# Kernel tuning notes

Measured on AMD Instinct MI355X. Metric: run time of the kernel, lower is better.

The kernel has to match this reference:

```python
import jax, jax.numpy as jnp
import numpy as np

T, B, D, H = 1024, 256, 128, 256

def setup_inputs() -> dict:
    key = jax.random.key(0)
    ks = jax.random.split(key, 6)
    s = 1.0 / np.sqrt(H)
    return {
        "x": jax.random.normal(ks[0], (T, B, D), dtype=jnp.float32),
        "delta_ts": jax.random.uniform(ks[1], (B, T), dtype=jnp.float32) * 10.0,  # elapsed times > 0
        "h0": jnp.zeros((B, H), dtype=jnp.float32),
        "c0": jnp.zeros((B, H), dtype=jnp.float32),
        "W": jax.random.normal(ks[2], (4 * H, D), dtype=jnp.float32) * s,
        "U": jax.random.normal(ks[3], (4 * H, H), dtype=jnp.float32) * s,
        "b": jnp.zeros((4 * H,), dtype=jnp.float32),
        "Wd": jax.random.normal(ks[4], (H, H), dtype=jnp.float32) * s,
        "bd": jnp.zeros((H,), dtype=jnp.float32),
    }

def reference(x, delta_ts, h0, c0, W, U, b, Wd, bd):
    """Time-aware LSTM (T-LSTM, Baytas et al. 2017) layer over time-major input.
    x: [T,B,D], delta_ts: [B,T]. Returns (outputs [T,B,H], (h,c))."""
    e = jnp.float32(np.e)

    def step(carry, inp):
        h, c = carry                 # [B,H] each
        xt, dt = inp                 # [B,D], [B]
        # memory decomposition with elapsed-time discount g(dt)=1/log(e+dt)
        Cs = jnp.tanh(c @ Wd.T + bd)                     # short-term memory [B,H]
        Cs_hat = Cs * (1.0 / jnp.log(e + dt))[:, None]   # discounted short-term
        c_star = c - Cs + Cs_hat                          # adjusted previous cell
        gates = xt @ W.T + h @ U.T + b                    # [B,4H]
        i, f, g, o = jnp.split(gates, 4, axis=-1)
        c_new = jax.nn.sigmoid(f) * c_star + jax.nn.sigmoid(i) * jnp.tanh(g)
        h_new = jax.nn.sigmoid(o) * jnp.tanh(c_new)
        return (h_new, c_new), h_new

    (h, c), outs = jax.lax.scan(step, (h0, c0), (x, delta_ts.T))
    return outs, h, c
```

## Files before the change

kernel.cpp:

```cpp
#include <hip/hip_runtime.h>

#define T_STEPS 1024
#define BATCH   256
#define DIM     128
#define HID     256
#define NSLICE  8
#define BT      16
#define NGROUP  (BATCH / BT)
#define NBLOCK  (NGROUP * NSLICE)
#define JW      (HID / NSLICE)

#define U_OFF    0
#define W_OFF    65536
#define WD_OFF   98304
#define H_OFF    114688
#define C_OFF    122880
#define GST_OFF  131072
#define CS0_OFF  139520
#define CS1_OFF  141632
#define SMEM_TOTAL 143744

typedef float f32x4 __attribute__((ext_vector_type(4)));
typedef short bf16x8 __attribute__((ext_vector_type(8)));

__device__ __forceinline__ unsigned short f2bf(float f) {
    union { float f; unsigned u; } v; v.f = f;
    unsigned r = (v.u + 0x7fffu + ((v.u >> 16) & 1u)) >> 16;
    return (unsigned short)r;
}
__device__ __forceinline__ float sigm(float v) { return 1.0f / (1.0f + __expf(-v)); }
__device__ __forceinline__ float tanh_fast(float v) {
    const float e = __expf(2.0f * v);
    return 1.0f - 2.0f / (e + 1.0f);
}

__global__ __launch_bounds__(512)
void tlstm_kernel(const float* __restrict__ x,
                  const float* __restrict__ dts,
                  const float* __restrict__ h0,
                  const float* __restrict__ c0,
                  const float* __restrict__ W,
                  const float* __restrict__ U,
                  const float* __restrict__ bvec,
                  const float* __restrict__ Wd,
                  const float* __restrict__ bd,
                  float* __restrict__ out,
                  unsigned long long* pbuf)
{
    extern __shared__ char smem[];
    float* gates_st = (float*)(smem + GST_OFF);
    float* cs0      = (float*)(smem + CS0_OFF);
    float* cs1      = (float*)(smem + CS1_OFF);

    const int tid = threadIdx.x;
    const int g  = blockIdx.x / NSLICE;
    const int s  = blockIdx.x % NSLICE;
    const int bb = g * BT;
    const int jb = s * JW;

    const int lane = tid & 63;
    const int wid  = tid >> 6;
    const int lrow = lane & 15;
    const int lkg  = lane >> 4;
    const int n0   = wid << 4;

    const int b_ = tid >> 5;
    const int jj = tid & 31;

    for (int idx = tid; idx < 128 * 256; idx += 512) {
        const int r = idx >> 8, k = idx & 255;
        const int urow = ((r >> 5) * HID) + jb + (r & 31);
        int bo = (r << 9) + (k << 1); bo ^= (r & 7) << 4;
        *(unsigned short*)(smem + U_OFF + bo) = f2bf(U[(size_t)urow * HID + k]);
    }
    for (int idx = tid; idx < 128 * 128; idx += 512) {
        const int r = idx >> 7, k = idx & 127;
        const int wrow = ((r >> 5) * HID) + jb + (r & 31);
        int bo = (r << 8) + (k << 1); bo ^= (r & 7) << 4;
        *(unsigned short*)(smem + W_OFF + bo) = f2bf(W[(size_t)wrow * DIM + k]);
    }
    for (int idx = tid; idx < 32 * 256; idx += 512) {
        const int r = idx >> 8, k = idx & 255;
        int bo = (r << 9) + (k << 1); bo ^= (r & 7) << 4;
        *(unsigned short*)(smem + WD_OFF + bo) = f2bf(Wd[(size_t)(jb + r) * HID + k]);
    }

    const float bI = bvec[jb + jj];
    const float bF = bvec[HID + jb + jj];
    const float bG = bvec[2 * HID + jb + jj];
    const float bO = bvec[3 * HID + jb + jj];
    const float bD = bd[jb + jj];

    float4 xr[8];
    float dt_cur;
    {
        const float* xp = x + ((size_t)0 * BATCH + bb + lrow) * DIM + (lkg << 3);
        #pragma unroll
        for (int kc = 0; kc < 4; ++kc) {
            xr[2 * kc]     = *(const float4*)(xp + kc * 32);
            xr[2 * kc + 1] = *(const float4*)(xp + kc * 32 + 4);
        }
        dt_cur = dts[(size_t)(bb + b_) * T_STEPS + 0];
    }

    float c_reg;
    {
        const float h0v = h0[(size_t)(bb + b_) * HID + jb + jj];
        const float c0v = c0[(size_t)(bb + b_) * HID + jb + jj];
        c_reg = c0v;
        const unsigned long long pv = (1ull << 32)
            | ((unsigned)f2bf(h0v) << 16) | (unsigned)f2bf(c0v);
        const size_t ei = (((size_t)0 * NGROUP + g) * NSLICE + s) * 512 + b_ * 32 + jj;
        __hip_atomic_store(pbuf + ei, pv, __ATOMIC_RELAXED, __HIP_MEMORY_SCOPE_AGENT);
    }

    for (int t = 0; t < T_STEPS; ++t) {
        const int cur = t & 1;

        bf16x8 xa[4];
        #pragma unroll
        for (int kc = 0; kc < 4; ++kc) {
            const float4 f0 = xr[2 * kc];
            const float4 f1 = xr[2 * kc + 1];
            bf16x8 a;
            a[0] = (short)f2bf(f0.x); a[1] = (short)f2bf(f0.y);
            a[2] = (short)f2bf(f0.z); a[3] = (short)f2bf(f0.w);
            a[4] = (short)f2bf(f1.x); a[5] = (short)f2bf(f1.y);
            a[6] = (short)f2bf(f1.z); a[7] = (short)f2bf(f1.w);
            xa[kc] = a;
        }
        f32x4 accX = {0.f, 0.f, 0.f, 0.f};
        {
            const int wr = n0 + lrow;
            #pragma unroll
            for (int kc = 0; kc < 4; ++kc) {
                int wo = (wr << 8) + ((kc * 32 + (lkg << 3)) << 1); wo ^= (wr & 7) << 4;
                const bf16x8 wv = *(const bf16x8*)(smem + W_OFF + wo);
                accX = __builtin_amdgcn_mfma_f32_16x16x32_bf16(xa[kc], wv, accX, 0, 0, 0);
            }
        }

        unsigned long long v[8];
        {
            const unsigned target = (unsigned)(t + 1);
            const unsigned long long* sp = pbuf
                + (((size_t)cur * NGROUP + g) * NSLICE + wid) * 512
                + ((lane >> 2) * 32 + ((lane & 3) << 3));
            bool ok;
            do {
                #pragma unroll
                for (int i = 0; i < 8; ++i)
                    v[i] = __hip_atomic_load(sp + i, __ATOMIC_RELAXED, __HIP_MEMORY_SCOPE_AGENT);
                ok = true;
                #pragma unroll
                for (int i = 0; i < 8; ++i)
                    ok = ok && ((unsigned)(v[i] >> 32) == target);
            } while (!__all((int)ok));
        }

        {
            bf16x8 hv, cv;
            #pragma unroll
            for (int i = 0; i < 8; ++i) {
                hv[i] = (short)((unsigned short)(v[i] >> 16));
                cv[i] = (short)((unsigned short)(v[i] & 0xffffu));
            }
            const int r  = lane >> 2;
            const int cb = (wid << 6) + ((lane & 3) << 4);
            int bo = (r << 9) + cb; bo ^= (r & 7) << 4;
            *(bf16x8*)(smem + H_OFF + bo) = hv;
            *(bf16x8*)(smem + C_OFF + bo) = cv;
        }
        __syncthreads();

        f32x4 accH = {0.f, 0.f, 0.f, 0.f};
        {
            const int wr = n0 + lrow;
            #pragma unroll
            for (int kc = 0; kc < 8; ++kc) {
                int ao = (lrow << 9) + ((kc * 32 + (lkg << 3)) << 1); ao ^= (lrow & 7) << 4;
                const bf16x8 av = *(const bf16x8*)(smem + H_OFF + ao);
                int uo = (wr << 9) + ((kc * 32 + (lkg << 3)) << 1); uo ^= (wr & 7) << 4;
                const bf16x8 uv = *(const bf16x8*)(smem + U_OFF + uo);
                accH = __builtin_amdgcn_mfma_f32_16x16x32_bf16(av, uv, accH, 0, 0, 0);
            }
        }
        if (wid < 4) {
            f32x4 accC = {0.f, 0.f, 0.f, 0.f};
            const int nt = wid >> 1;
            const int kh = wid & 1;
            const int wr = (nt << 4) + lrow;
            #pragma unroll
            for (int kc = 0; kc < 4; ++kc) {
                const int kk = kh * 4 + kc;
                int ao = (lrow << 9) + ((kk * 32 + (lkg << 3)) << 1); ao ^= (lrow & 7) << 4;
                const bf16x8 av = *(const bf16x8*)(smem + C_OFF + ao);
                int wo = (wr << 9) + ((kk * 32 + (lkg << 3)) << 1); wo ^= (wr & 7) << 4;
                const bf16x8 wv = *(const bf16x8*)(smem + WD_OFF + wo);
                accC = __builtin_amdgcn_mfma_f32_16x16x32_bf16(av, wv, accC, 0, 0, 0);
            }
            float* dst = kh ? cs1 : cs0;
            #pragma unroll
            for (int i = 0; i < 4; ++i)
                dst[((lkg << 2) + i) * 33 + (nt << 4) + lrow] = accC[i];
        }
        #pragma unroll
        for (int i = 0; i < 4; ++i)
            gates_st[((lkg << 2) + i) * 132 + n0 + lrow] = accX[i] + accH[i];

        __syncthreads();

        float cn, hn;
        {
            const float ipre = gates_st[b_ * 132 + jj]      + bI;
            const float fpre = gates_st[b_ * 132 + 32 + jj] + bF;
            const float gpre = gates_st[b_ * 132 + 64 + jj] + bG;
            const float opre = gates_st[b_ * 132 + 96 + jj] + bO;
            const float cspre = cs0[b_ * 33 + jj] + cs1[b_ * 33 + jj] + bD;
            const float gdt  = 1.0f / __logf(2.718281828459045f + dt_cur);
            const float Cs    = tanh_fast(cspre);
            const float cstar = c_reg - Cs + Cs * gdt;
            cn = sigm(fpre) * cstar + sigm(ipre) * tanh_fast(gpre);
            hn = sigm(opre) * tanh_fast(cn);
            c_reg = cn;
        }

        if (t == T_STEPS - 1) {
            out[((size_t)t * BATCH + bb + b_) * HID + jb + jj] = hn;
            const size_t base = (size_t)T_STEPS * BATCH * HID;
            out[base + (size_t)(bb + b_) * HID + jb + jj] = hn;
            out[base + (size_t)BATCH * HID + (size_t)(bb + b_) * HID + jb + jj] = cn;
            break;
        }

        {
            const unsigned long long pv = ((unsigned long long)(unsigned)(t + 2) << 32)
                | ((unsigned)f2bf(hn) << 16) | (unsigned)f2bf(cn);
            const size_t ei = (((size_t)(cur ^ 1) * NGROUP + g) * NSLICE + s) * 512
                            + b_ * 32 + jj;
            __hip_atomic_store(pbuf + ei, pv, __ATOMIC_RELAXED, __HIP_MEMORY_SCOPE_AGENT);
        }

        out[((size_t)t * BATCH + bb + b_) * HID + jb + jj] = hn;
        {
            const float* xp = x + ((size_t)(t + 1) * BATCH + bb + lrow) * DIM + (lkg << 3);
            #pragma unroll
            for (int kc = 0; kc < 4; ++kc) {
                xr[2 * kc]     = *(const float4*)(xp + kc * 32);
                xr[2 * kc + 1] = *(const float4*)(xp + kc * 32 + 4);
            }
            dt_cur = dts[(size_t)(bb + b_) * T_STEPS + (t + 1)];
        }
    }
}

extern "C" void kernel_launch(void* const* d_in, const int* in_sizes, int n_in,
                              void* d_out, int out_size, void* d_ws, size_t ws_size,
                              hipStream_t stream) {
    (void)in_sizes; (void)n_in; (void)out_size; (void)ws_size;
    const float* x   = (const float*)d_in[0];
    const float* dts = (const float*)d_in[1];
    const float* h0  = (const float*)d_in[2];
    const float* c0  = (const float*)d_in[3];
    const float* W   = (const float*)d_in[4];
    const float* U   = (const float*)d_in[5];
    const float* bv  = (const float*)d_in[6];
    const float* Wd  = (const float*)d_in[7];
    const float* bd  = (const float*)d_in[8];
    float* out = (float*)d_out;

    unsigned long long* pbuf = (unsigned long long*)d_ws;
    const size_t pbuf_bytes = 2ull * NGROUP * NSLICE * 512 * 8;

    hipMemsetAsync(pbuf, 0, pbuf_bytes, stream);
    hipFuncSetAttribute((const void*)tlstm_kernel,
                        hipFuncAttributeMaxDynamicSharedMemorySize, SMEM_TOTAL);
    tlstm_kernel<<<dim3(NBLOCK), dim3(512), SMEM_TOTAL, stream>>>(
        x, dts, h0, c0, W, U, bv, Wd, bd, out, pbuf);
}
```

Measured before the change: 5.439 ms.

## Interleave two batch sub-tiles per block to overlap cross-block sync latency

```diff
diff --git a/kernel.cpp b/kernel.cpp
--- a/kernel.cpp
+++ b/kernel.cpp
@@ -4,10 +4,10 @@
 #define BATCH   256
 #define DIM     128
 #define HID     256
+#define NGP     8
 #define NSLICE  8
+#define NBLOCK  (NGP * NSLICE)
 #define BT      16
-#define NGROUP  (BATCH / BT)
-#define NBLOCK  (NGROUP * NSLICE)
 #define JW      (HID / NSLICE)
 
 #define U_OFF    0
@@ -20,6 +20,11 @@
 #define CS1_OFF  141632
 #define SMEM_TOTAL 143744
 
+#define SLICE_CH 512
+#define ST_CH    (8 * SLICE_CH)
+#define GP_CH    (2 * ST_CH)
+#define BUF_CH   (NGP * GP_CH)
+
 typedef float f32x4 __attribute__((ext_vector_type(4)));
 typedef short bf16x8 __attribute__((ext_vector_type(8)));
 
@@ -32,6 +37,17 @@
 __device__ __forceinline__ float tanh_fast(float v) {
     const float e = __expf(2.0f * v);
     return 1.0f - 2.0f / (e + 1.0f);
+}
+__device__ __forceinline__ void lgkm_bar() {
+    asm volatile("s_waitcnt lgkmcnt(0)" ::: "memory");
+    __builtin_amdgcn_s_barrier();
+    __builtin_amdgcn_sched_barrier(0);
+}
+__device__ __forceinline__ void probe8(const unsigned long long* sp, unsigned long long v[8]) {
+    #pragma unroll
+    for (int i = 0; i < 8; ++i)
+        v[i] = __hip_atomic_load(sp + i, __ATOMIC_RELAXED, __HIP_MEMORY_SCOPE_AGENT);
+    __builtin_amdgcn_sched_barrier(0);
 }
 
 __global__ __launch_bounds__(512)
@@ -52,12 +68,7 @@
     float* cs0      = (float*)(smem + CS0_OFF);
     float* cs1      = (float*)(smem + CS1_OFF);
 
-    const int tid = threadIdx.x;
-    const int g  = blockIdx.x / NSLICE;
-    const int s  = blockIdx.x % NSLICE;
-    const int bb = g * BT;
-    const int jb = s * JW;
-
+    const int tid  = threadIdx.x;
     const int lane = tid & 63;
     const int wid  = tid >> 6;
     const int lrow = lane & 15;
@@ -67,6 +78,10 @@
     const int b_ = tid >> 5;
     const int jj = tid & 31;
 
+    const int gp = blockIdx.x >> 3;
+    const int s  = blockIdx.x & 7;
+    const int jb = s * JW;
+
     for (int idx = tid; idx < 128 * 256; idx += 512) {
         const int r = idx >> 8, k = idx & 255;
         const int urow = ((r >> 5) * HID) + jb + (r & 31);
@@ -91,166 +106,186 @@
     const float bO = bvec[3 * HID + jb + jj];
     const float bD = bd[jb + jj];
 
-    float4 xr[8];
-    float dt_cur;
-    {
-        const float* xp = x + ((size_t)0 * BATCH + bb + lrow) * DIM + (lkg << 3);
+    float4 xr[2][8];
+    float dtv[2], dtn[2];
+    #pragma unroll
+    for (int st = 0; st < 2; ++st) {
+        const float* xp = x + ((size_t)0 * BATCH + gp * 32 + st * 16 + lrow) * DIM + (lkg << 3);
         #pragma unroll
         for (int kc = 0; kc < 4; ++kc) {
-            xr[2 * kc]     = *(const float4*)(xp + kc * 32);
-            xr[2 * kc + 1] = *(const float4*)(xp + kc * 32 + 4);
+            xr[st][2 * kc]     = *(const float4*)(xp + kc * 32);
+            xr[st][2 * kc + 1] = *(const float4*)(xp + kc * 32 + 4);
         }
-        dt_cur = dts[(size_t)(bb + b_) * T_STEPS + 0];
-    }
-
-    float c_reg;
-    {
-        const float h0v = h0[(size_t)(bb + b_) * HID + jb + jj];
-        const float c0v = c0[(size_t)(bb + b_) * HID + jb + jj];
-        c_reg = c0v;
+        dtv[st] = dts[(size_t)(gp * 32 + st * 16 + b_) * T_STEPS + 0];
+        dtn[st] = dtv[st];
+    }
+
+    float c_reg[2];
+    #pragma unroll
+    for (int st = 0; st < 2; ++st) {
+        const int rowg = gp * 32 + st * 16 + b_;
+        const float h0v = h0[(size_t)rowg * HID + jb + jj];
+        const float c0v = c0[(size_t)rowg * HID + jb + jj];
+        c_reg[st] = c0v;
         const unsigned long long pv = (1ull << 32)
             | ((unsigned)f2bf(h0v) << 16) | (unsigned)f2bf(c0v);
-        const size_t ei = (((size_t)0 * NGROUP + g) * NSLICE + s) * 512 + b_ * 32 + jj;
+        const int ei = gp * GP_CH + st * ST_CH + s * SLICE_CH + b_ * 32 + jj;
         __hip_atomic_store(pbuf + ei, pv, __ATOMIC_RELAXED, __HIP_MEMORY_SCOPE_AGENT);
     }
+    __syncthreads();
+
+    unsigned long long v[2][8];
+    probe8(pbuf + gp * GP_CH + 0 * ST_CH + wid * SLICE_CH + lane * 8, v[0]);
 
     for (int t = 0; t < T_STEPS; ++t) {
         const int cur = t & 1;
-
-        bf16x8 xa[4];
         #pragma unroll
-        for (int kc = 0; kc < 4; ++kc) {
-            const float4 f0 = xr[2 * kc];
-            const float4 f1 = xr[2 * kc + 1];
-            bf16x8 a;
-            a[0] = (short)f2bf(f0.x); a[1] = (short)f2bf(f0.y);
-            a[2] = (short)f2bf(f0.z); a[3] = (short)f2bf(f0.w);
-            a[4] = (short)f2bf(f1.x); a[5] = (short)f2bf(f1.y);
-            a[6] = (short)f2bf(f1.z); a[7] = (short)f2bf(f1.w);
-            xa[kc] = a;
-        }
-        f32x4 accX = {0.f, 0.f, 0.f, 0.f};
-        {
-            const int wr = n0 + lrow;
+        for (int st = 0; st < 2; ++st) {
+            const unsigned target = (unsigned)(t + 1);
+            const unsigned long long* sp = pbuf + cur * BUF_CH + gp * GP_CH
+                                         + st * ST_CH + wid * SLICE_CH + lane * 8;
+            for (;;) {
+                bool ok = true;
+                #pragma unroll
+                for (int i = 0; i < 8; ++i)
+                    ok = ok && ((unsigned)(v[st][i] >> 32) == target);
+                if (__all((int)ok)) break;
+                probe8(sp, v[st]);
+            }
+            {
+                bf16x8 hv, cv;
+                #pragma unroll
+                for (int i = 0; i < 8; ++i) {
+                    hv[i] = (short)((unsigned short)(v[st][i] >> 16));
+                    cv[i] = (short)((unsigned short)(v[st][i] & 0xffffu));
+                }
+                const int r  = lane >> 2;
+                const int cb = (wid << 6) + ((lane & 3) << 4);
+                int bo = (r << 9) + cb; bo ^= (r & 7) << 4;
+                *(bf16x8*)(smem + H_OFF + bo) = hv;
+                *(bf16x8*)(smem + C_OFF + bo) = cv;
+            }
+            lgkm_bar();
+
+            if (st == 0) {
+                probe8(pbuf + cur * BUF_CH + gp * GP_CH + ST_CH
+                       + wid * SLICE_CH + lane * 8, v[1]);
+            } else if (t < T_STEPS - 1) {
+                probe8(pbuf + (cur ^ 1) * BUF_CH + gp * GP_CH
+                       + wid * SLICE_CH + lane * 8, v[0]);
+            }
+
+            bf16x8 xa[4];
             #pragma unroll
             for (int kc = 0; kc < 4; ++kc) {
-                int wo = (wr << 8) + ((kc * 32 + (lkg << 3)) << 1); wo ^= (wr & 7) << 4;
-                const bf16x8 wv = *(const bf16x8*)(smem + W_OFF + wo);
-                accX = __builtin_amdgcn_mfma_f32_16x16x32_bf16(xa[kc], wv, accX, 0, 0, 0);
-            }
-        }
-
-        unsigned long long v[8];
-        {
-            const unsigned target = (unsigned)(t + 1);
-            const unsigned long long* sp = pbuf
-                + (((size_t)cur * NGROUP + g) * NSLICE + wid) * 512
-                + ((lane >> 2) * 32 + ((lane & 3) << 3));
-            bool ok;
-            do {
-                #pragma unroll
-                for (int i = 0; i < 8; ++i)
-                    v[i] = __hip_atomic_load(sp + i, __ATOMIC_RELAXED, __HIP_MEMORY_SCOPE_AGENT);
-                ok = true;
-                #pragma unroll
-                for (int i = 0; i < 8; ++i)
-                    ok = ok && ((unsigned)(v[i] >> 32) == target);
-            } while (!__all((int)ok));
-        }
-
-        {
-            bf16x8 hv, cv;
-            #pragma unroll
-            for (int i = 0; i < 8; ++i) {
-                hv[i] = (short)((unsigned short)(v[i] >> 16));
-                cv[i] = (short)((unsigned short)(v[i] & 0xffffu));
-            }
-            const int r  = lane >> 2;
-            const int cb = (wid << 6) + ((lane & 3) << 4);
-            int bo = (r << 9) + cb; bo ^= (r & 7) << 4;
-            *(bf16x8*)(smem + H_OFF + bo) = hv;
-            *(bf16x8*)(smem + C_OFF + bo) = cv;
-        }
-        __syncthreads();
-
-        f32x4 accH = {0.f, 0.f, 0.f, 0.f};
-        {
-            const int wr = n0 + lrow;
-            #pragma unroll
-            for (int kc = 0; kc < 8; ++kc) {
-                int ao = (lrow << 9) + ((kc * 32 + (lkg << 3)) << 1); ao ^= (lrow & 7) << 4;
-                const bf16x8 av = *(const bf16x8*)(smem + H_OFF + ao);
-                int uo = (wr << 9) + ((kc * 32 + (lkg << 3)) << 1); uo ^= (wr & 7) << 4;
-                const bf16x8 uv = *(const bf16x8*)(smem + U_OFF + uo);
-                accH = __builtin_amdgcn_mfma_f32_16x16x32_bf16(av, uv, accH, 0, 0, 0);
-            }
-        }
-        if (wid < 4) {
-            f32x4 accC = {0.f, 0.f, 0.f, 0.f};
-            const int nt = wid >> 1;
-            const int kh = wid & 1;
-            const int wr = (nt << 4) + lrow;
-            #pragma unroll
-            for (int kc = 0; kc < 4; ++kc) {
-                const int kk = kh * 4 + kc;
-                int ao = (lrow << 9) + ((kk * 32 + (lkg << 3)) << 1); ao ^= (lrow & 7) << 4;
-                const bf16x8 av = *(const bf16x8*)(smem + C_OFF + ao);
-                int wo = (wr << 9) + ((kk * 32 + (lkg << 3)) << 1); wo ^= (wr & 7) << 4;
-                const bf16x8 wv = *(const bf16x8*)(smem + WD_OFF + wo);
-                accC = __builtin_amdgcn_mfma_f32_16x16x32_bf16(av, wv, accC, 0, 0, 0);
-            }
-            float* dst = kh ? cs1 : cs0;
+                const float4 f0 = xr[st][2 * kc];
+                const float4 f1 = xr[st][2 * kc + 1];
+                bf16x8 a;
+                a[0] = (short)f2bf(f0.x); a[1] = (short)f2bf(f0.y);
+                a[2] = (short)f2bf(f0.z); a[3] = (short)f2bf(f0.w);
+                a[4] = (short)f2bf(f1.x); a[5] = (short)f2bf(f1.y);
+                a[6] = (short)f2bf(f1.z); a[7] = (short)f2bf(f1.w);
+                xa[kc] = a;
+            }
+            if (st == 1 && t < T_STEPS - 1) {
+                #pragma unroll
+                for (int ss = 0; ss < 2; ++ss) {
+                    const float* xp = x + ((size_t)(t + 1) * BATCH + gp * 32 + ss * 16 + lrow) * DIM + (lkg << 3);
+                    #pragma unroll
+                    for (int kc = 0; kc < 4; ++kc) {
+                        xr[ss][2 * kc]     = *(const float4*)(xp + kc * 32);
+                        xr[ss][2 * kc + 1] = *(const float4*)(xp + kc * 32 + 4);
+                    }
+                    dtn[ss] = dts[(size_t)(gp * 32 + ss * 16 + b_) * T_STEPS + (t + 1)];
+                }
+            }
+
+            f32x4 accX = {0.f, 0.f, 0.f, 0.f};
+            f32x4 accH = {0.f, 0.f, 0.f, 0.f};
+            {
+                const int wr = n0 + lrow;
+                #pragma unroll
+                for (int kc = 0; kc < 4; ++kc) {
+                    int wo = (wr << 8) + ((kc * 32 + (lkg << 3)) << 1); wo ^= (wr & 7) << 4;
+                    const bf16x8 wv = *(const bf16x8*)(smem + W_OFF + wo);
+                    accX = __builtin_amdgcn_mfma_f32_16x16x32_bf16(xa[kc], wv, accX, 0, 0, 0);
+                }
+                #pragma unroll
+                for (int kc = 0; kc < 8; ++kc) {
+                    int ao = (lrow << 9) + ((kc * 32 + (lkg << 3)) << 1); ao ^= (lrow & 7) << 4;
+                    const bf16x8 av = *(const bf16x8*)(smem + H_OFF + ao);
+                    int uo = (wr << 9) + ((kc * 32 + (lkg << 3)) << 1); uo ^= (wr & 7) << 4;
+                    const bf16x8 uv = *(const bf16x8*)(smem + U_OFF + uo);
+                    accH = __builtin_amdgcn_mfma_f32_16x16x32_bf16(av, uv, accH, 0, 0, 0);
+                }
+            }
+            if (wid < 4) {
+                f32x4 accC = {0.f, 0.f, 0.f, 0.f};
+                const int nt = wid >> 1;
+                const int kh = wid & 1;
+                const int wr = (nt << 4) + lrow;
+                #pragma unroll
+                for (int kc = 0; kc < 4; ++kc) {
+                    const int kk = kh * 4 + kc;
+                    int ao = (lrow << 9) + ((kk * 32 + (lkg << 3)) << 1); ao ^= (lrow & 7) << 4;
+                    const bf16x8 av = *(const bf16x8*)(smem + C_OFF + ao);
+                    int wo = (wr << 9) + ((kk * 32 + (lkg << 3)) << 1); wo ^= (wr & 7) << 4;
+                    const bf16x8 wv = *(const bf16x8*)(smem + WD_OFF + wo);
+                    accC = __builtin_amdgcn_mfma_f32_16x16x32_bf16(av, wv, accC, 0, 0, 0);
+                }
+                float* dst = kh ? cs1 : cs0;
+                #pragma unroll
+                for (int i = 0; i < 4; ++i)
+                    dst[((lkg << 2) + i) * 33 + (nt << 4) + lrow] = accC[i];
+            }
             #pragma unroll
             for (int i = 0; i < 4; ++i)
-                dst[((lkg << 2) + i) * 33 + (nt << 4) + lrow] = accC[i];
+                gates_st[((lkg << 2) + i) * 132 + n0 + lrow] = accX[i] + accH[i];
+
+            lgkm_bar();
+
+            float cn, hn;
+            {
+                const float ipre = gates_st[b_ * 132 + jj]      + bI;
+                const float fpre = gates_st[b_ * 132 + 32 + jj] + bF;
+                const float gpre = gates_st[b_ * 132 + 64 + jj] + bG;
+                const float opre = gates_st[b_ * 132 + 96 + jj] + bO;
+                const float cspre = cs0[b_ * 33 + jj] + cs1[b_ * 33 + jj] + bD;
+                const float gdt  = 1.0f / __logf(2.718281828459045f + dtv[st]);
+                const float Cs    = tanh_fast(cspre);
+                const float cstar = c_reg[st] - Cs + Cs * gdt;
+                cn = sigm(fpre) * cstar + sigm(ipre) * tanh_fast(gpre);
+                hn = sigm(opre) * tanh_fast(cn);
+                c_reg[st] = cn;
+            }
+
+            const int rowg = gp * 32 + st * 16 + b_;
+            if (t == T_STEPS - 1) {
+                out[((size_t)t * BATCH + rowg) * HID + jb + jj] = hn;
+                const size_t base = (size_t)T_STEPS * BATCH * HID;
+                out[base + (size_t)rowg * HID + jb + jj] = hn;
+                out[base + (size_t)BATCH * HID + (size_t)rowg * HID + jb + jj] = cn;
+            } else {
+                const unsigned long long pv = ((unsigned long long)(unsigned)(t + 2) << 32)
+                    | ((unsigned)f2bf(hn) << 16) | (unsigned)f2bf(cn);
+                const int ei = (cur ^ 1) * BUF_CH + gp * GP_CH + st * ST_CH
+                             + s * SLICE_CH + b_ * 32 + jj;
+                __hip_atomic_store(pbuf + ei, pv, __ATOMIC_RELAXED, __HIP_MEMORY_SCOPE_AGENT);
+                out[((size_t)t * BATCH + rowg) * HID + jb + jj] = hn;
+            }
+
+            if (st == 1 && t < T_STEPS - 1) {
+                bool okA = true;
+                #pragma unroll
+                for (int i = 0; i < 8; ++i)
+                    okA = okA && ((unsigned)(v[0][i] >> 32) == (unsigned)(t + 2));
+                if (!__all((int)okA))
+                    probe8(pbuf + (cur ^ 1) * BUF_CH + gp * GP_CH
+                           + wid * SLICE_CH + lane * 8, v[0]);
+            }
         }
-        #pragma unroll
-        for (int i = 0; i < 4; ++i)
-            gates_st[((lkg << 2) + i) * 132 + n0 + lrow] = accX[i] + accH[i];
-
-        __syncthreads();
-
-        float cn, hn;
-        {
-            const float ipre = gates_st[b_ * 132 + jj]      + bI;
-            const float fpre = gates_st[b_ * 132 + 32 + jj] + bF;
-            const float gpre = gates_st[b_ * 132 + 64 + jj] + bG;
-            const float opre = gates_st[b_ * 132 + 96 + jj] + bO;
-            const float cspre = cs0[b_ * 33 + jj] + cs1[b_ * 33 + jj] + bD;
-            const float gdt  = 1.0f / __logf(2.718281828459045f + dt_cur);
-            const float Cs    = tanh_fast(cspre);
-            const float cstar = c_reg - Cs + Cs * gdt;
-            cn = sigm(fpre) * cstar + sigm(ipre) * tanh_fast(gpre);
-            hn = sigm(opre) * tanh_fast(cn);
-            c_reg = cn;
-        }
-
-        if (t == T_STEPS - 1) {
-            out[((size_t)t * BATCH + bb + b_) * HID + jb + jj] = hn;
-            const size_t base = (size_t)T_STEPS * BATCH * HID;
-            out[base + (size_t)(bb + b_) * HID + jb + jj] = hn;
-            out[base + (size_t)BATCH * HID + (size_t)(bb + b_) * HID + jb + jj] = cn;
-            break;
-        }
-
-        {
-            const unsigned long long pv = ((unsigned long long)(unsigned)(t + 2) << 32)
-                | ((unsigned)f2bf(hn) << 16) | (unsigned)f2bf(cn);
-            const size_t ei = (((size_t)(cur ^ 1) * NGROUP + g) * NSLICE + s) * 512
-                            + b_ * 32 + jj;
-            __hip_atomic_store(pbuf + ei, pv, __ATOMIC_RELAXED, __HIP_MEMORY_SCOPE_AGENT);
-        }
-
-        out[((size_t)t * BATCH + bb + b_) * HID + jb + jj] = hn;
-        {
-            const float* xp = x + ((size_t)(t + 1) * BATCH + bb + lrow) * DIM + (lkg << 3);
-            #pragma unroll
-            for (int kc = 0; kc < 4; ++kc) {
-                xr[2 * kc]     = *(const float4*)(xp + kc * 32);
-                xr[2 * kc + 1] = *(const float4*)(xp + kc * 32 + 4);
-            }
-            dt_cur = dts[(size_t)(bb + b_) * T_STEPS + (t + 1)];
-        }
+        dtv[0] = dtn[0];
+        dtv[1] = dtn[1];
     }
 }
 
@@ -270,9 +305,8 @@
     float* out = (float*)d_out;
 
     unsigned long long* pbuf = (unsigned long long*)d_ws;
-    const size_t pbuf_bytes = 2ull * NGROUP * NSLICE * 512 * 8;
-
-    hipMemsetAsync(pbuf, 0, pbuf_bytes, stream);
+
+    hipMemsetAsync(pbuf, 0, (size_t)2 * BUF_CH * 8, stream);
     hipFuncSetAttribute((const void*)tlstm_kernel,
                         hipFuncAttributeMaxDynamicSharedMemorySize, SMEM_TOTAL);
     tlstm_kernel<<<dim3(NBLOCK), dim3(512), SMEM_TOTAL, stream>>>(
```

Measured after the change: 9.187 ms. 68.9% more time.

## Give each block a full batch tile and drop the inter-block flag sync

Applied to the files above, without the earlier changes.

```diff
diff --git a/kernel.cpp b/kernel.cpp
--- a/kernel.cpp
+++ b/kernel.cpp
@@ -4,21 +4,14 @@
 #define BATCH   256
 #define DIM     128
 #define HID     256
-#define NSLICE  8
 #define BT      16
-#define NGROUP  (BATCH / BT)
-#define NBLOCK  (NGROUP * NSLICE)
-#define JW      (HID / NSLICE)
-
-#define U_OFF    0
-#define W_OFF    65536
-#define WD_OFF   98304
-#define H_OFF    114688
-#define C_OFF    122880
-#define GST_OFF  131072
-#define CS0_OFF  139520
-#define CS1_OFF  141632
-#define SMEM_TOTAL 143744
+#define NBLK    (BATCH / BT)
+
+#define WD_OFF 0
+#define H_OFF  131072
+#define C_OFF  139264
+#define X_OFF  147456
+#define SMEM_TOTAL 155648
 
 typedef float f32x4 __attribute__((ext_vector_type(4)));
 typedef short bf16x8 __attribute__((ext_vector_type(8)));
@@ -28,13 +21,26 @@
     unsigned r = (v.u + 0x7fffu + ((v.u >> 16) & 1u)) >> 16;
     return (unsigned short)r;
 }
+__device__ __forceinline__ bf16x8 cvt8(float4 a, float4 b) {
+    bf16x8 r;
+    r[0] = (short)f2bf(a.x); r[1] = (short)f2bf(a.y);
+    r[2] = (short)f2bf(a.z); r[3] = (short)f2bf(a.w);
+    r[4] = (short)f2bf(b.x); r[5] = (short)f2bf(b.y);
+    r[6] = (short)f2bf(b.z); r[7] = (short)f2bf(b.w);
+    return r;
+}
 __device__ __forceinline__ float sigm(float v) { return 1.0f / (1.0f + __expf(-v)); }
 __device__ __forceinline__ float tanh_fast(float v) {
     const float e = __expf(2.0f * v);
     return 1.0f - 2.0f / (e + 1.0f);
 }
-
-__global__ __launch_bounds__(512)
+__device__ __forceinline__ void lgkm_bar() {
+    asm volatile("s_waitcnt lgkmcnt(0)" ::: "memory");
+    __builtin_amdgcn_s_barrier();
+    __builtin_amdgcn_sched_barrier(0);
+}
+
+__global__ __launch_bounds__(512, 1)
 void tlstm_kernel(const float* __restrict__ x,
                   const float* __restrict__ dts,
                   const float* __restrict__ h0,
@@ -44,220 +50,198 @@
                   const float* __restrict__ bvec,
                   const float* __restrict__ Wd,
                   const float* __restrict__ bd,
-                  float* __restrict__ out,
-                  unsigned long long* pbuf)
+                  float* __restrict__ out)
 {
     extern __shared__ char smem[];
-    float* gates_st = (float*)(smem + GST_OFF);
-    float* cs0      = (float*)(smem + CS0_OFF);
-    float* cs1      = (float*)(smem + CS1_OFF);
-
-    const int tid = threadIdx.x;
-    const int g  = blockIdx.x / NSLICE;
-    const int s  = blockIdx.x % NSLICE;
-    const int bb = g * BT;
-    const int jb = s * JW;
-
+    const int tid  = threadIdx.x;
     const int lane = tid & 63;
-    const int wid  = tid >> 6;
+    const int w    = tid >> 6;
     const int lrow = lane & 15;
     const int lkg  = lane >> 4;
-    const int n0   = wid << 4;
-
-    const int b_ = tid >> 5;
-    const int jj = tid & 31;
-
-    for (int idx = tid; idx < 128 * 256; idx += 512) {
-        const int r = idx >> 8, k = idx & 255;
-        const int urow = ((r >> 5) * HID) + jb + (r & 31);
-        int bo = (r << 9) + (k << 1); bo ^= (r & 7) << 4;
-        *(unsigned short*)(smem + U_OFF + bo) = f2bf(U[(size_t)urow * HID + k]);
-    }
-    for (int idx = tid; idx < 128 * 128; idx += 512) {
-        const int r = idx >> 7, k = idx & 127;
-        const int wrow = ((r >> 5) * HID) + jb + (r & 31);
-        int bo = (r << 8) + (k << 1); bo ^= (r & 7) << 4;
-        *(unsigned short*)(smem + W_OFF + bo) = f2bf(W[(size_t)wrow * DIM + k]);
-    }
-    for (int idx = tid; idx < 32 * 256; idx += 512) {
+    const int bb   = blockIdx.x * BT;
+
+    for (int idx = tid; idx < 256 * 256; idx += 512) {
         const int r = idx >> 8, k = idx & 255;
         int bo = (r << 9) + (k << 1); bo ^= (r & 7) << 4;
-        *(unsigned short*)(smem + WD_OFF + bo) = f2bf(Wd[(size_t)(jb + r) * HID + k]);
-    }
-
-    const float bI = bvec[jb + jj];
-    const float bF = bvec[HID + jb + jj];
-    const float bG = bvec[2 * HID + jb + jj];
-    const float bO = bvec[3 * HID + jb + jj];
-    const float bD = bd[jb + jj];
-
-    float4 xr[8];
-    float dt_cur;
+        *(unsigned short*)(smem + WD_OFF + bo) = f2bf(Wd[(size_t)r * HID + k]);
+    }
+    for (int idx = tid; idx < 16 * 256; idx += 512) {
+        const int r = idx >> 8, k = idx & 255;
+        int bo = (r << 9) + (k << 1); bo ^= (r & 7) << 4;
+        *(unsigned short*)(smem + H_OFF + bo) = f2bf(h0[(size_t)(bb + r) * HID + k]);
+        *(unsigned short*)(smem + C_OFF + bo) = f2bf(c0[(size_t)(bb + r) * HID + k]);
+    }
     {
-        const float* xp = x + ((size_t)0 * BATCH + bb + lrow) * DIM + (lkg << 3);
+        const int r = tid >> 5, c4 = (tid & 31) * 4;
+        const float4 f = *(const float4*)(x + ((size_t)0 * BATCH + bb + r) * DIM + c4);
+        const unsigned long long pk =
+              (unsigned long long)f2bf(f.x)
+            | ((unsigned long long)f2bf(f.y) << 16)
+            | ((unsigned long long)f2bf(f.z) << 32)
+            | ((unsigned long long)f2bf(f.w) << 48);
+        int bo = (r << 8) + (c4 << 1); bo ^= (r & 7) << 4;
+        *(unsigned long long*)(smem + X_OFF + bo) = pk;
+    }
+
+    bf16x8 UB[8][8];
+    bf16x8 WB[8][4];
+    #pragma unroll
+    for (int nt = 0; nt < 8; ++nt) {
+        const int q = nt >> 1, hf = nt & 1;
+        const int grow = q * HID + w * 32 + hf * 16 + lrow;
+        #pragma unroll
+        for (int kc = 0; kc < 8; ++kc) {
+            const float* up = U + (size_t)grow * HID + kc * 32 + lkg * 8;
+            UB[nt][kc] = cvt8(*(const float4*)up, *(const float4*)(up + 4));
+        }
         #pragma unroll
         for (int kc = 0; kc < 4; ++kc) {
-            xr[2 * kc]     = *(const float4*)(xp + kc * 32);
-            xr[2 * kc + 1] = *(const float4*)(xp + kc * 32 + 4);
-        }
-        dt_cur = dts[(size_t)(bb + b_) * T_STEPS + 0];
-    }
-
-    float c_reg;
-    {
-        const float h0v = h0[(size_t)(bb + b_) * HID + jb + jj];
-        const float c0v = c0[(size_t)(bb + b_) * HID + jb + jj];
-        c_reg = c0v;
-        const unsigned long long pv = (1ull << 32)
-            | ((unsigned)f2bf(h0v) << 16) | (unsigned)f2bf(c0v);
-        const size_t ei = (((size_t)0 * NGROUP + g) * NSLICE + s) * 512 + b_ * 32 + jj;
-        __hip_atomic_store(pbuf + ei, pv, __ATOMIC_RELAXED, __HIP_MEMORY_SCOPE_AGENT);
-    }
-
+            const float* wp = W + (size_t)grow * DIM + kc * 32 + lkg * 8;
+            WB[nt][kc] = cvt8(*(const float4*)wp, *(const float4*)(wp + 4));
+        }
+    }
+
+    float bI[2], bF[2], bG[2], bO[2], bD2[2];
+    #pragma unroll
+    for (int hf = 0; hf < 2; ++hf) {
+        const int j = w * 32 + hf * 16 + lrow;
+        bI[hf]  = bvec[j];
+        bF[hf]  = bvec[HID + j];
+        bG[hf]  = bvec[2 * HID + j];
+        bO[hf]  = bvec[3 * HID + j];
+        bD2[hf] = bd[j];
+    }
+
+    float c_reg[2][4];
+    #pragma unroll
+    for (int hf = 0; hf < 2; ++hf)
+        #pragma unroll
+        for (int i = 0; i < 4; ++i)
+            c_reg[hf][i] = c0[(size_t)(bb + lkg * 4 + i) * HID + w * 32 + hf * 16 + lrow];
+
+    float dt_r[4], dt_n[4];
+    #pragma unroll
+    for (int i = 0; i < 4; ++i)
+        dt_r[i] = dts[(size_t)(bb + lkg * 4 + i) * T_STEPS + 0];
+
+    __syncthreads();
+
+    float4 xpre;
+
+    #pragma unroll 1
     for (int t = 0; t < T_STEPS; ++t) {
-        const int cur = t & 1;
-
-        bf16x8 xa[4];
+        const int xb = t & 1;
+
+        const int tn = (t + 1 < T_STEPS) ? t + 1 : t;
+        {
+            const int r = tid >> 5, c4 = (tid & 31) * 4;
+            xpre = *(const float4*)(x + ((size_t)tn * BATCH + bb + r) * DIM + c4);
+            #pragma unroll
+            for (int i = 0; i < 4; ++i)
+                dt_n[i] = dts[(size_t)(bb + lkg * 4 + i) * T_STEPS + tn];
+        }
+
+        f32x4 accG[4][2];
+        f32x4 accC[2];
+        #pragma unroll
+        for (int q = 0; q < 4; ++q)
+            #pragma unroll
+            for (int hf = 0; hf < 2; ++hf)
+                accG[q][hf] = (f32x4){0.f, 0.f, 0.f, 0.f};
+        accC[0] = (f32x4){0.f, 0.f, 0.f, 0.f};
+        accC[1] = (f32x4){0.f, 0.f, 0.f, 0.f};
+
         #pragma unroll
         for (int kc = 0; kc < 4; ++kc) {
-            const float4 f0 = xr[2 * kc];
-            const float4 f1 = xr[2 * kc + 1];
-            bf16x8 a;
-            a[0] = (short)f2bf(f0.x); a[1] = (short)f2bf(f0.y);
-            a[2] = (short)f2bf(f0.z); a[3] = (short)f2bf(f0.w);
-            a[4] = (short)f2bf(f1.x); a[5] = (short)f2bf(f1.y);
-            a[6] = (short)f2bf(f1.z); a[7] = (short)f2bf(f1.w);
-            xa[kc] = a;
-        }
-        f32x4 accX = {0.f, 0.f, 0.f, 0.f};
+            int bo = (lrow << 8) + ((kc * 32 + lkg * 8) << 1); bo ^= (lrow & 7) << 4;
+            const bf16x8 xa = *(const bf16x8*)(smem + X_OFF + xb * 4096 + bo);
+            #pragma unroll
+            for (int q = 0; q < 4; ++q)
+                #pragma unroll
+                for (int hf = 0; hf < 2; ++hf)
+                    accG[q][hf] = __builtin_amdgcn_mfma_f32_16x16x32_bf16(
+                        xa, WB[q * 2 + hf][kc], accG[q][hf], 0, 0, 0);
+        }
+        #pragma unroll
+        for (int kc = 0; kc < 8; ++kc) {
+            int bo = (lrow << 9) + ((kc * 32 + lkg * 8) << 1); bo ^= (lrow & 7) << 4;
+            const bf16x8 ha = *(const bf16x8*)(smem + H_OFF + bo);
+            #pragma unroll
+            for (int q = 0; q < 4; ++q)
+                #pragma unroll
+                for (int hf = 0; hf < 2; ++hf)
+                    accG[q][hf] = __builtin_amdgcn_mfma_f32_16x16x32_bf16(
+                        ha, UB[q * 2 + hf][kc], accG[q][hf], 0, 0, 0);
+        }
+        #pragma unroll
+        for (int kc = 0; kc < 8; ++kc) {
+            int bo = (lrow << 9) + ((kc * 32 + lkg * 8) << 1); bo ^= (lrow & 7) << 4;
+            const bf16x8 ca = *(const bf16x8*)(smem + C_OFF + bo);
+            #pragma unroll
+            for (int hf = 0; hf < 2; ++hf) {
+                const int wr = w * 32 + hf * 16 + lrow;
+                int wo = (wr << 9) + ((kc * 32 + lkg * 8) << 1); wo ^= (wr & 7) << 4;
+                const bf16x8 wd = *(const bf16x8*)(smem + WD_OFF + wo);
+                accC[hf] = __builtin_amdgcn_mfma_f32_16x16x32_bf16(ca, wd, accC[hf], 0, 0, 0);
+            }
+        }
+        lgkm_bar();
+
         {
-            const int wr = n0 + lrow;
-            #pragma unroll
-            for (int kc = 0; kc < 4; ++kc) {
-                int wo = (wr << 8) + ((kc * 32 + (lkg << 3)) << 1); wo ^= (wr & 7) << 4;
-                const bf16x8 wv = *(const bf16x8*)(smem + W_OFF + wo);
-                accX = __builtin_amdgcn_mfma_f32_16x16x32_bf16(xa[kc], wv, accX, 0, 0, 0);
+            const int r = tid >> 5, c4 = (tid & 31) * 4;
+            const unsigned long long pk =
+                  (unsigned long long)f2bf(xpre.x)
+                | ((unsigned long long)f2bf(xpre.y) << 16)
+                | ((unsigned long long)f2bf(xpre.z) << 32)
+                | ((unsigned long long)f2bf(xpre.w) << 48);
+            int bo = (r << 8) + (c4 << 1); bo ^= (r & 7) << 4;
+            *(unsigned long long*)(smem + X_OFF + (xb ^ 1) * 4096 + bo) = pk;
+        }
+
+        float gdt[4];
+        #pragma unroll
+        for (int i = 0; i < 4; ++i)
+            gdt[i] = 1.0f / __logf(2.718281828459045f + dt_r[i]);
+
+        #pragma unroll
+        for (int hf = 0; hf < 2; ++hf) {
+            const int j = w * 32 + hf * 16 + lrow;
+            #pragma unroll
+            for (int i = 0; i < 4; ++i) {
+                const int rb = lkg * 4 + i;
+                const float ipre = accG[0][hf][i] + bI[hf];
+                const float fpre = accG[1][hf][i] + bF[hf];
+                const float gpre = accG[2][hf][i] + bG[hf];
+                const float opre = accG[3][hf][i] + bO[hf];
+                const float Cs    = tanh_fast(accC[hf][i] + bD2[hf]);
+                const float cstar = c_reg[hf][i] - Cs + Cs * gdt[i];
+                const float cn = sigm(fpre) * cstar + sigm(ipre) * tanh_fast(gpre);
+                const float hn = sigm(opre) * tanh_fast(cn);
+                c_reg[hf][i] = cn;
+
+                int bo = (rb << 9) + (j << 1); bo ^= (rb & 7) << 4;
+                *(unsigned short*)(smem + H_OFF + bo) = f2bf(hn);
+                *(unsigned short*)(smem + C_OFF + bo) = f2bf(cn);
+
+                out[((size_t)t * BATCH + bb + rb) * HID + j] = hn;
+                if (t == T_STEPS - 1) {
+                    const size_t base = (size_t)T_STEPS * BATCH * HID;
+                    out[base + (size_t)(bb + rb) * HID + j] = hn;
+                    out[base + (size_t)BATCH * HID + (size_t)(bb + rb) * HID + j] = cn;
+                }
             }
         }
-
-        unsigned long long v[8];
-        {
-            const unsigned target = (unsigned)(t + 1);
-            const unsigned long long* sp = pbuf
-                + (((size_t)cur * NGROUP + g) * NSLICE + wid) * 512
-                + ((lane >> 2) * 32 + ((lane & 3) << 3));
-            bool ok;
-            do {
-                #pragma unroll
-                for (int i = 0; i < 8; ++i)
-                    v[i] = __hip_atomic_load(sp + i, __ATOMIC_RELAXED, __HIP_MEMORY_SCOPE_AGENT);
-                ok = true;
-                #pragma unroll
-                for (int i = 0; i < 8; ++i)
-                    ok = ok && ((unsigned)(v[i] >> 32) == target);
-            } while (!__all((int)ok));
-        }
-
-        {
-            bf16x8 hv, cv;
-            #pragma unroll
-            for (int i = 0; i < 8; ++i) {
-                hv[i] = (short)((unsigned short)(v[i] >> 16));
-                cv[i] = (short)((unsigned short)(v[i] & 0xffffu));
-            }
-            const int r  = lane >> 2;
-            const int cb = (wid << 6) + ((lane & 3) << 4);
-            int bo = (r << 9) + cb; bo ^= (r & 7) << 4;
-            *(bf16x8*)(smem + H_OFF + bo) = hv;
-            *(bf16x8*)(smem + C_OFF + bo) = cv;
-        }
-        __syncthreads();
-
-        f32x4 accH = {0.f, 0.f, 0.f, 0.f};
-        {
-            const int wr = n0 + lrow;
-            #pragma unroll
-            for (int kc = 0; kc < 8; ++kc) {
-                int ao = (lrow << 9) + ((kc * 32 + (lkg << 3)) << 1); ao ^= (lrow & 7) << 4;
-                const bf16x8 av = *(const bf16x8*)(smem + H_OFF + ao);
-                int uo = (wr << 9) + ((kc * 32 + (lkg << 3)) << 1); uo ^= (wr & 7) << 4;
-                const bf16x8 uv = *(const bf16x8*)(smem + U_OFF + uo);
-                accH = __builtin_amdgcn_mfma_f32_16x16x32_bf16(av, uv, accH, 0, 0, 0);
-            }
-        }
-        if (wid < 4) {
-            f32x4 accC = {0.f, 0.f, 0.f, 0.f};
-            const int nt = wid >> 1;
-            const int kh = wid & 1;
-            const int wr = (nt << 4) + lrow;
-            #pragma unroll
-            for (int kc = 0; kc < 4; ++kc) {
-                const int kk = kh * 4 + kc;
-                int ao = (lrow << 9) + ((kk * 32 + (lkg << 3)) << 1); ao ^= (lrow & 7) << 4;
-                const bf16x8 av = *(const bf16x8*)(smem + C_OFF + ao);
-                int wo = (wr << 9) + ((kk * 32 + (lkg << 3)) << 1); wo ^= (wr & 7) << 4;
-                const bf16x8 wv = *(const bf16x8*)(smem + WD_OFF + wo);
-                accC = __builtin_amdgcn_mfma_f32_16x16x32_bf16(av, wv, accC, 0, 0, 0);
-            }
-            float* dst = kh ? cs1 : cs0;
-            #pragma unroll
-            for (int i = 0; i < 4; ++i)
-                dst[((lkg << 2) + i) * 33 + (nt << 4) + lrow] = accC[i];
-        }
-        #pragma unroll
-        for (int i = 0; i < 4; ++i)
-            gates_st[((lkg << 2) + i) * 132 + n0 + lrow] = accX[i] + accH[i];
-
-        __syncthreads();
-
-        float cn, hn;
-        {
-            const float ipre = gates_st[b_ * 132 + jj]      + bI;
-            const float fpre = gates_st[b_ * 132 + 32 + jj] + bF;
-            const float gpre = gates_st[b_ * 132 + 64 + jj] + bG;
-            const float opre = gates_st[b_ * 132 + 96 + jj] + bO;
-            const float cspre = cs0[b_ * 33 + jj] + cs1[b_ * 33 + jj] + bD;
-            const float gdt  = 1.0f / __logf(2.718281828459045f + dt_cur);
-            const float Cs    = tanh_fast(cspre);
-            const float cstar = c_reg - Cs + Cs * gdt;
-            cn = sigm(fpre) * cstar + sigm(ipre) * tanh_fast(gpre);
-            hn = sigm(opre) * tanh_fast(cn);
-            c_reg = cn;
-        }
-
-        if (t == T_STEPS - 1) {
-            out[((size_t)t * BATCH + bb + b_) * HID + jb + jj] = hn;
-            const size_t base = (size_t)T_STEPS * BATCH * HID;
-            out[base + (size_t)(bb + b_) * HID + jb + jj] = hn;
-            out[base + (size_t)BATCH * HID + (size_t)(bb + b_) * HID + jb + jj] = cn;
-            break;
-        }
-
-        {
-            const unsigned long long pv = ((unsigned long long)(unsigned)(t + 2) << 32)
-                | ((unsigned)f2bf(hn) << 16) | (unsigned)f2bf(cn);
-            const size_t ei = (((size_t)(cur ^ 1) * NGROUP + g) * NSLICE + s) * 512
-                            + b_ * 32 + jj;
-            __hip_atomic_store(pbuf + ei, pv, __ATOMIC_RELAXED, __HIP_MEMORY_SCOPE_AGENT);
-        }
-
-        out[((size_t)t * BATCH + bb + b_) * HID + jb + jj] = hn;
-        {
-            const float* xp = x + ((size_t)(t + 1) * BATCH + bb + lrow) * DIM + (lkg << 3);
-            #pragma unroll
-            for (int kc = 0; kc < 4; ++kc) {
-                xr[2 * kc]     = *(const float4*)(xp + kc * 32);
-                xr[2 * kc + 1] = *(const float4*)(xp + kc * 32 + 4);
-            }
-            dt_cur = dts[(size_t)(bb + b_) * T_STEPS + (t + 1)];
-        }
+        #pragma unroll
+        for (int i = 0; i < 4; ++i) dt_r[i] = dt_n[i];
+
+        lgkm_bar();
     }
 }
 
 extern "C" void kernel_launch(void* const* d_in, const int* in_sizes, int n_in,
                               void* d_out, int out_size, void* d_ws, size_t ws_size,
                               hipStream_t stream) {
-    (void)in_sizes; (void)n_in; (void)out_size; (void)ws_size;
+    (void)in_sizes; (void)n_in; (void)out_size; (void)d_ws; (void)ws_size;
     const float* x   = (const float*)d_in[0];
     const float* dts = (const float*)d_in[1];
     const float* h0  = (const float*)d_in[2];
@@ -269,12 +253,8 @@
     const float* bd  = (const float*)d_in[8];
     float* out = (float*)d_out;
 
-    unsigned long long* pbuf = (unsigned long long*)d_ws;
-    const size_t pbuf_bytes = 2ull * NGROUP * NSLICE * 512 * 8;
-
-    hipMemsetAsync(pbuf, 0, pbuf_bytes, stream);
     hipFuncSetAttribute((const void*)tlstm_kernel,
                         hipFuncAttributeMaxDynamicSharedMemorySize, SMEM_TOTAL);
-    tlstm_kernel<<<dim3(NBLOCK), dim3(512), SMEM_TOTAL, stream>>>(
-        x, dts, h0, c0, W, U, bv, Wd, bd, out, pbuf);
-}
+    tlstm_kernel<<<dim3(NBLK), dim3(512), SMEM_TOTAL, stream>>>(
+        x, dts, h0, c0, W, U, bv, Wd, bd, out);
+}
```

New measurement: 20.15 ms (median of 2 runs). 3.71x slower.
